# Kernel tuning notes

Measured on AMD Instinct MI355X. Metric: run time of the kernel, lower is better.

## Reference

```python
import jax, jax.numpy as jnp
import numpy as np

B, N_UNK, M_KNOWN = 8, 8192, 2048
C1, C2 = 256, 256
MLP = [512, 256, 256]
K_ENC = 32
D = MLP[-1]


def setup_inputs() -> dict:
    key = jax.random.key(0)
    ks = jax.random.split(key, 16)
    return {
        "unknown": jax.random.normal(ks[0], (B, N_UNK, 3), jnp.float32),
        "known": jax.random.normal(ks[1], (B, M_KNOWN, 3), jnp.float32),
        "unknow_feats": jax.random.normal(ks[2], (B, C1, N_UNK), jnp.float32),
        "known_feats": jax.random.normal(ks[3], (B, C2, M_KNOWN), jnp.float32),
        "conv_w1": jax.random.normal(ks[4], (MLP[1], MLP[0]), jnp.float32) * 0.05,
        "conv_b1": jnp.zeros((MLP[1],), jnp.float32),
        "bn_g1": jnp.ones((MLP[1],), jnp.float32),
        "bn_b1": jnp.zeros((MLP[1],), jnp.float32),
        "bn_m1": jax.random.normal(ks[5], (MLP[1],), jnp.float32) * 0.01,
        "bn_v1": jax.random.uniform(ks[6], (MLP[1],), jnp.float32, 0.5, 1.5),
        "conv_w2": jax.random.normal(ks[7], (MLP[2], MLP[1]), jnp.float32) * 0.05,
        "conv_b2": jnp.zeros((MLP[2],), jnp.float32),
        "bn_g2": jnp.ones((MLP[2],), jnp.float32),
        "bn_b2": jnp.zeros((MLP[2],), jnp.float32),
        "bn_m2": jax.random.normal(ks[8], (MLP[2],), jnp.float32) * 0.01,
        "bn_v2": jax.random.uniform(ks[9], (MLP[2],), jnp.float32, 0.5, 1.5),
        "enc_codewords": jax.random.normal(ks[10], (K_ENC, D), jnp.float32) * float(1.0 / np.sqrt(K_ENC * D)),
        "enc_scale": jax.random.uniform(ks[11], (K_ENC,), jnp.float32, -1.0, 0.0),
        "lin_w": jax.random.normal(ks[12], (D, D * K_ENC), jnp.float32) * 0.02,
        "lin_b": jnp.zeros((D,), jnp.float32),
    }


def _conv_bn_relu(x, w, b, g, beta, mean, var):
    # 1x1 conv over (B,C,N) == channel GEMM, then BN (inference form), then ReLU
    x = jnp.einsum("oc,bcn->bon", w, x) + b[None, :, None]
    x = g[None, :, None] * (x - mean[None, :, None]) * jax.lax.rsqrt(var + 1e-5)[None, :, None] + beta[None, :, None]
    return jax.nn.relu(x)


def reference(unknown, known, unknow_feats, known_feats,
              conv_w1, conv_b1, bn_g1, bn_b1, bn_m1, bn_v1,
              conv_w2, conv_b2, bn_g2, bn_b2, bn_m2, bn_v2,
              enc_codewords, enc_scale, lin_w, lin_b):
    # ---- three_nn: 3 nearest known points for each unknown point ----
    x2 = jnp.sum(unknown * unknown, axis=-1)            # (B,n)
    y2 = jnp.sum(known * known, axis=-1)                # (B,m)
    d2 = x2[:, :, None] - 2.0 * jnp.einsum("bnc,bmc->bnm", unknown, known) + y2[:, None, :]
    dist = jnp.sqrt(jnp.maximum(d2, 1e-12))             # (B,n,m) Euclidean
    neg_d, idx = jax.lax.top_k(-dist, 3)                # 3 smallest
    dist3 = -neg_d                                      # (B,n,3)
    dist_recip = 1.0 / (dist3 + 1e-8)
    weight = dist_recip / jnp.sum(dist_recip, axis=2, keepdims=True)
    # ---- three_interpolate: gather + weighted sum ----
    gathered = jax.vmap(lambda f, i: f[:, i])(known_feats, idx)   # (B,C2,n,3)
    interp = jnp.einsum("bcnk,bnk->bcn", gathered, weight)        # (B,C2,n)
    feats = jnp.concatenate([interp, unknow_feats], axis=1)       # (B,C2+C1,n)
    # ---- SharedMLP (two 1x1 conv + BN + ReLU layers) ----
    h = _conv_bn_relu(feats, conv_w1, conv_b1, bn_g1, bn_b1, bn_m1, bn_v1)
    h = _conv_bn_relu(h, conv_w2, conv_b2, bn_g2, bn_b2, bn_m2, bn_v2)   # (B,D,n)
    # ---- Encoding layer (soft dictionary assignment, residual aggregate) ----
    X = jnp.swapaxes(h, 1, 2)                                     # (B,n,D)
    c2 = jnp.sum(enc_codewords * enc_codewords, axis=-1)          # (K,)
    xn2 = jnp.sum(X * X, axis=-1)                                 # (B,n)
    # scaled_l2: s_k * ||x - c_k||^2 without materializing (B,n,K,D) residuals
    sl = enc_scale[None, None, :] * (xn2[:, :, None] - 2.0 * jnp.einsum("bnd,kd->bnk", X, enc_codewords) + c2[None, None, :])
    A = jax.nn.softmax(sl, axis=-1)                               # (B,n,K)
    E = jnp.einsum("bnk,bnd->bkd", A, X) - jnp.sum(A, axis=1)[:, :, None] * enc_codewords[None]
    E = jax.nn.relu(E).reshape(E.shape[0], -1)                    # (B,K*D)
    E = E / jnp.maximum(jnp.linalg.norm(E, axis=1, keepdims=True), 1e-12)  # F.normalize
    ctx = jax.nn.sigmoid(E @ lin_w.T + lin_b)                     # (B,D)
    # ---- channel-attention fusion ----
    return h * ctx[:, :, None]                                    # (B,D,n)
```

## Files before the change

### kernel.cpp

```cpp
#include <hip/hip_runtime.h>
#include <stdint.h>

typedef unsigned short u16;
typedef unsigned int u32;
typedef __attribute__((ext_vector_type(8))) short short8;
typedef __attribute__((ext_vector_type(4))) float f32x4;
typedef __attribute__((ext_vector_type(4))) u32 u32x4;

#define B_ 8
#define N_ 8192
#define M_ 2048
#define DD 256
#define KENC 32

#define SC1 0
#define SH1 256
#define SC2 512
#define SH2 768
#define C2OFF 1024
#define SOFF 1056
#define RNOFF 1088

#define OFF_IDX3   0ull
#define OFF_W3     786432ull
#define OFF_FT     1572864ull
#define OFF_H1T    68681728ull
#define OFF_ERELU  102236160ull
#define OFF_PART   102498304ull
#define OFF_CONSTS 102760448ull
#define OFF_CTX    102768640ull
#define OFF_W1D    102776832ull
#define OFF_W2D    103038976ull
#define OFF_CWD    103170048ull
#define OFF_FLAG   103186432ull

__device__ __forceinline__ float bf2f(u16 v){ return __uint_as_float(((u32)v)<<16); }
__device__ __forceinline__ u16 f2bf(float f){
  u32 x = __float_as_uint(f);
  return (u16)((x + 0x7FFFu + ((x>>16)&1u)) >> 16);
}
__device__ __forceinline__ float ldf(const void* p, size_t i, int f){
  return f ? ((const float*)p)[i] : bf2f(((const u16*)p)[i]);
}
__device__ __forceinline__ void gl_lds16(const u16* g, u16* l){
  __builtin_amdgcn_global_load_lds(
      (const __attribute__((address_space(1))) void*)g,
      (__attribute__((address_space(3))) void*)l, 16, 0, 0);
}

__global__ __launch_bounds__(256) void k_detect(const void* v1, int* flagp){
  __shared__ int cntb, cntf;
  int t = threadIdx.x;
  if (t==0){ cntb=0; cntf=0; }
  __syncthreads();
  float vb = bf2f(((const u16*)v1)[t]);
  if (!(vb > 0.4f && vb < 1.6f)) atomicAdd(&cntb, 1);
  if (t < 64){
    float vf = ((const float*)v1)[t];
    if (!(vf > 0.4f && vf < 1.6f)) atomicAdd(&cntf, 1);
  }
  __syncthreads();
  if (t==0) flagp[0] = (cntb > 0 && cntf == 0) ? 1 : 0;
}

__global__ __launch_bounds__(256) void k_convert(
    const void* w1, const void* w2, const void* cwsrc, const int* __restrict__ flagp,
    u16* __restrict__ W1d, u16* __restrict__ W2d, u16* __restrict__ CWd){
  int id = blockIdx.x*256 + threadIdx.x;
  int f = flagp[0];
  if (id < 131072){
    W1d[id] = f ? f2bf(((const float*)w1)[id]) : ((const u16*)w1)[id];
  } else if (id < 196608){
    int j = id - 131072;
    W2d[j] = f ? f2bf(((const float*)w2)[j]) : ((const u16*)w2)[j];
  } else if (id < 204800){
    int j = id - 196608;
    CWd[j] = f ? f2bf(((const float*)cwsrc)[j]) : ((const u16*)cwsrc)[j];
  }
}

__global__ __launch_bounds__(256) void k0_setup(
    const void* cb1, const void* g1, const void* be1, const void* m1, const void* v1,
    const void* cb2, const void* g2, const void* be2, const void* m2, const void* v2,
    const u16* __restrict__ CWd, const void* es, const int* __restrict__ flagp,
    float* __restrict__ consts){
  int t = threadIdx.x;
  int f = flagp[0];
  {
    float g = ldf(g1,t,f), be = ldf(be1,t,f), m = ldf(m1,t,f), v = ldf(v1,t,f), cb = ldf(cb1,t,f);
    float r = 1.f/sqrtf(v + 1e-5f);
    float sc = g*r;
    consts[SC1+t] = sc; consts[SH1+t] = (cb-m)*sc + be;
  }
  {
    float g = ldf(g2,t,f), be = ldf(be2,t,f), m = ldf(m2,t,f), v = ldf(v2,t,f), cb = ldf(cb2,t,f);
    float r = 1.f/sqrtf(v + 1e-5f);
    float sc = g*r;
    consts[SC2+t] = sc; consts[SH2+t] = (cb-m)*sc + be;
  }
  if (t < KENC){
    float s = 0.f;
    for (int d=0; d<DD; d++){ float c = bf2f(CWd[t*DD+d]); s = fmaf(c,c,s); }
    consts[C2OFF+t] = s;
    consts[SOFF+t]  = ldf(es,t,f);
  }
}

__device__ __forceinline__ float k1_dist2(float x2, float u2x, float u2y, float u2z, float4 km){
  float dot2 = __fadd_rn(__fadd_rn(__fmul_rn(u2x,km.x), __fmul_rn(u2y,km.y)), __fmul_rn(u2z,km.z));
  return __fadd_rn(__fsub_rn(x2, dot2), km.w);
}
__global__ __launch_bounds__(256) void k1_three_nn(
    const void* unknown, const void* known, const int* __restrict__ flagp,
    int* __restrict__ idx3, float* __restrict__ w3){
  __shared__ float4 kp[M_];
  int b = blockIdx.y, t = threadIdx.x;
  int f = flagp[0];
  for (int i=t; i<M_; i+=256){
    size_t o = ((size_t)b*M_ + i)*3;
    float x = ldf(known,o,f), y = ldf(known,o+1,f), z = ldf(known,o+2,f);
    float y2 = __fadd_rn(__fadd_rn(__fmul_rn(x,x), __fmul_rn(y,y)), __fmul_rn(z,z));
    kp[i] = make_float4(x,y,z,y2);
  }
  __syncthreads();
  int qq = t >> 2, sl = t & 3;
  int pid = blockIdx.x*64 + qq;
  size_t uo = ((size_t)b*N_ + pid)*3;
  float ux=ldf(unknown,uo,f), uy=ldf(unknown,uo+1,f), uz=ldf(unknown,uo+2,f);
  float x2 = __fadd_rn(__fadd_rn(__fmul_rn(ux,ux), __fmul_rn(uy,uy)), __fmul_rn(uz,uz));
  float u2x = ux+ux, u2y = uy+uy, u2z = uz+uz;
  float b0=3.4e38f, b1=3.4e38f, b2v=3.4e38f;
  const float4* kpl = kp + sl;
  for (int j0=0; j0<512; j0+=4){
    #pragma unroll
    for (int u=0; u<4; u++){
      float4 km = kpl[(j0+u)*4];
      float d2 = k1_dist2(x2,u2x,u2y,u2z,km);
      float t0 = fminf(b0, d2);
      float t1 = __builtin_amdgcn_fmed3f(b0, b1, d2);
      float t2 = __builtin_amdgcn_fmed3f(b1, b2v, d2);
      b0=t0; b1=t1; b2v=t2;
    }
  }
  #pragma unroll
  for (int st=1; st<4; st<<=1){
    float o0=__shfl_xor(b0,st,64), o1=__shfl_xor(b1,st,64), o2=__shfl_xor(b2v,st,64);
    float dv[3] = {o0,o1,o2};
    #pragma unroll
    for (int e=0; e<3; e++){
      float dd = dv[e];
      float t0 = fminf(b0, dd);
      float t1 = __builtin_amdgcn_fmed3f(b0, b1, dd);
      float t2 = __builtin_amdgcn_fmed3f(b1, b2v, dd);
      b0=t0; b1=t1; b2v=t2;
    }
  }
  float T = b2v;
  float e0=3.4e38f, e1=3.4e38f, e2=3.4e38f;
  int i0=0x7fffffff, i1=0x7fffffff, i2=0x7fffffff;
  for (int j0=0; j0<512; j0+=4){
    float d[4];
    #pragma unroll
    for (int u=0; u<4; u++){
      float4 km = kpl[(j0+u)*4];
      d[u] = k1_dist2(x2,u2x,u2y,u2z,km);
    }
    float gmin = fminf(fminf(d[0],d[1]), fminf(d[2],d[3]));
    if (__builtin_expect(gmin <= T, 0)){
      #pragma unroll
      for (int u=0; u<4; u++){
        float dd = d[u];
        if (dd <= T){
          int m = (j0+u)*4 + sl;
          bool lt0 = (dd < e0) || (dd == e0 && m < i0);
          bool lt1 = (dd < e1) || (dd == e1 && m < i1);
          bool lt2 = (dd < e2) || (dd == e2 && m < i2);
          float n2 = lt1 ? e1 : (lt2 ? dd : e2);  int ni2 = lt1 ? i1 : (lt2 ? m : i2);
          float n1 = lt0 ? e0 : (lt1 ? dd : e1);  int ni1 = lt0 ? i0 : (lt1 ? m : i1);
          e0 = lt0 ? dd : e0;  i0 = lt0 ? m : i0;
          e1 = n1; i1 = ni1; e2 = n2; i2 = ni2;
        }
      }
    }
  }
  #pragma unroll
  for (int st=1; st<4; st<<=1){
    float o0=__shfl_xor(e0,st,64), o1=__shfl_xor(e1,st,64), o2=__shfl_xor(e2,st,64);
    int   j0=__shfl_xor(i0,st,64), j1=__shfl_xor(i1,st,64), j2=__shfl_xor(i2,st,64);
    float dv[3] = {o0,o1,o2}; int jv[3] = {j0,j1,j2};
    #pragma unroll
    for (int e=0; e<3; e++){
      float dd = dv[e]; int jj = jv[e];
      bool lt2 = (dd < e2) || (dd == e2 && jj < i2);
      if (lt2){
        bool lt0 = (dd < e0) || (dd == e0 && jj < i0);
        bool lt1 = (dd < e1) || (dd == e1 && jj < i1);
        if (lt0){ e2=e1;i2=i1; e1=e0;i1=i0; e0=dd;i0=jj; }
        else if (lt1){ e2=e1;i2=i1; e1=dd;i1=jj; }
        else { e2=dd; i2=jj; }
      }
    }
  }
  if (sl == 0){
    float da = __fsqrt_rn(fmaxf(e0,1e-12f));
    float db = __fsqrt_rn(fmaxf(e1,1e-12f));
    float dc = __fsqrt_rn(fmaxf(e2,1e-12f));
    float r0 = __fdiv_rn(1.f, __fadd_rn(da,1e-8f));
    float r1 = __fdiv_rn(1.f, __fadd_rn(db,1e-8f));
    float r2 = __fdiv_rn(1.f, __fadd_rn(dc,1e-8f));
    float rs = __fadd_rn(__fadd_rn(r0,r1),r2);
    size_t o = ((size_t)b*N_ + pid)*3;
    idx3[o]=i0; idx3[o+1]=i1; idx3[o+2]=i2;
    w3[o]=__fdiv_rn(r0,rs); w3[o+1]=__fdiv_rn(r1,rs); w3[o+2]=__fdiv_rn(r2,rs);
  }
}

__global__ __launch_bounds__(256) void k2_interp(
    const void* kf, const int* __restrict__ idx3,
    const float* __restrict__ w3, const int* __restrict__ flagp, u16* __restrict__ Ft){
  __shared__ u16 Ls[M_*8];
  int ct = blockIdx.x;
  int rg = blockIdx.y;
  int b = blockIdx.z, t = threadIdx.x;
  int f = flagp[0];
  for (int cp=0; cp<4; cp++){
    int c0 = ct*8 + cp*2;
    size_t base0 = ((size_t)b*DD + c0)*M_;
    size_t base1 = base0 + M_;
    for (int i=t; i<M_; i+=256){
      float f0 = ldf(kf, base0+i, f);
      float f1 = ldf(kf, base1+i, f);
      u32 w = (u32)f2bf(f0) | ((u32)f2bf(f1)<<16);
      *(u32*)(Ls + i*8 + cp*2) = w;
    }
  }
  __syncthreads();
  for (int rep=rg*8; rep<rg*8+8; rep++){
    int pid = rep*256 + t;
    size_t o3 = ((size_t)b*N_ + pid)*3;
    int ia = idx3[o3], ib = idx3[o3+1], ic = idx3[o3+2];
    float wa = w3[o3], wb = w3[o3+1], wc = w3[o3+2];
    short8 va = *(const short8*)(Ls + ia*8);
    short8 vb = *(const short8*)(Ls + ib*8);
    short8 vc = *(const short8*)(Ls + ic*8);
    u32x4 pk;
    #pragma unroll
    for (int cq=0; cq<4; cq++){
      float fa0 = bf2f((u16)va[cq*2]),   fb0 = bf2f((u16)vb[cq*2]),   fc0 = bf2f((u16)vc[cq*2]);
      float fa1 = bf2f((u16)va[cq*2+1]), fb1 = bf2f((u16)vb[cq*2+1]), fc1 = bf2f((u16)vc[cq*2+1]);
      float v0 = fmaf(wc, fc0, fmaf(wb, fb0, wa*fa0));
      float v1 = fmaf(wc, fc1, fmaf(wb, fb1, wa*fa1));
      pk[cq] = (u32)f2bf(v0) | ((u32)f2bf(v1)<<16);
    }
    *(u32x4*)(Ft + ((size_t)b*N_ + pid)*512 + ct*8) = pk;
  }
}

__global__ __launch_bounds__(256) void k2b_transpose_uf(
    const void* uf, const int* __restrict__ flagp, u16* __restrict__ Ft){
  __shared__ u16 Ls[64*72];
  int bx = blockIdx.x, cy = blockIdx.y, b = blockIdx.z, t = threadIdx.x;
  int f = flagp[0];
  {
    int n = t & 63, cg = t >> 6;
    for (int i=0; i<16; i++){
      int c = cg*16 + i;
      Ls[n*72 + c] = f2bf(ldf(uf, ((size_t)b*DD + cy*64 + c)*N_ + bx*64 + n, f));
    }
  }
  __syncthreads();
  int nl = t>>2, cc = t&3;
  u16* dst = Ft + ((size_t)b*N_ + bx*64 + nl)*512 + 256 + cy*64 + cc*16;
  *(u32x4*)dst     = *(const u32x4*)(Ls + nl*72 + cc*16);
  *(u32x4*)(dst+8) = *(const u32x4*)(Ls + nl*72 + cc*16 + 8);
}

__global__ __launch_bounds__(256) void gemm_bn_relu(
    const u16* __restrict__ W, const u16* __restrict__ Fin,
    const float* __restrict__ consts, int sc_off, int sh_off,
    u16* __restrict__ Out, int K){
  __shared__ u16 SM[17408];
  u16* As = SM; u16* Bs = SM + 8192;
  int b = blockIdx.z, ot = blockIdx.y*128, nt = blockIdx.x*128;
  int t = threadIdx.x, wave = t>>6, lane = t&63, ln = lane&15, quad = lane>>4;
  int wo = (wave&1)*64, wn = (wave>>1)*64;
  f32x4 acc[4][4];
  #pragma unroll
  for (int i=0;i<4;i++)
    #pragma unroll
    for (int j=0;j<4;j++) acc[i][j] = (f32x4)0.f;
  const u16* Wp = W + (size_t)ot*K;
  const u16* Fp = Fin + ((size_t)b*N_ + nt)*K;
  for (int kk=0; kk<K; kk+=64){
    #pragma unroll
    for (int i=0;i<4;i++){
      int c = wave*256 + i*64 + lane;
      int r = c>>3, k8 = (c&7) ^ (r&7);
      const u16* gA = Wp + (size_t)r*K + kk + k8*8;
      const u16* gB = Fp + (size_t)r*K + kk + k8*8;
      gl_lds16(gA, As + (size_t)(wave*256 + i*64)*8);
      gl_lds16(gB, Bs + (size_t)(wave*256 + i*64)*8);
    }
    __syncthreads();
    #pragma unroll
    for (int kh=0; kh<2; kh++){
      short8 af[4], bfr[4];
      #pragma unroll
      for (int i=0;i<4;i++){
        int R = wo + i*16 + ln, C = kh*4 + quad;
        af[i] = *(const short8*)(As + (size_t)(R*8 + (C^(R&7)))*8);
      }
      #pragma unroll
      for (int j=0;j<4;j++){
        int R = wn + j*16 + ln, C = kh*4 + quad;
        bfr[j] = *(const short8*)(Bs + (size_t)(R*8 + (C^(R&7)))*8);
      }
      #pragma unroll
      for (int i=0;i<4;i++)
        #pragma unroll
        for (int j=0;j<4;j++)
          acc[i][j] = __builtin_amdgcn_mfma_f32_16x16x32_bf16(af[i], bfr[j], acc[i][j], 0,0,0);
    }
    __syncthreads();
  }
  u16* Cs = SM;
  #pragma unroll
  for (int i=0;i<4;i++){
    #pragma unroll
    for (int r=0;r<4;r++){
      int ol = wo + i*16 + quad*4 + r;
      float sc = consts[sc_off + ot + ol], sh = consts[sh_off + ot + ol];
      #pragma unroll
      for (int j=0;j<4;j++){
        float v = fmaxf(fmaf(acc[i][j][r], sc, sh), 0.f);
        Cs[(wn + j*16 + ln)*136 + ol] = f2bf(v);
      }
    }
  }
  __syncthreads();
  int nl = t>>1, half = t&1;
  u16* dst = Out + ((size_t)b*N_ + nt + nl)*256 + ot + half*64;
  const u16* srcr = Cs + nl*136 + half*64;
  #pragma unroll
  for (int c=0;c<8;c++)
    *(u32x4*)(dst + c*8) = *(const u32x4*)(srcr + c*8);
}

__global__ __launch_bounds__(256, 6) void k5_enc_partial(
    const u16* __restrict__ X, const u16* __restrict__ cw,
    const float* __restrict__ consts, float* __restrict__ Epart,
    float* __restrict__ Asum){
  __shared__ u16 Xs[64*256];
  __shared__ float A_lds[64*32];
  int g = blockIdx.x, b = blockIdx.y, t = threadIdx.x;
  int wave = t>>6, lane = t&63, ln = lane&15, quad = lane>>4;
  int ka = lane>>1, h = lane&1;
  int dbase = wave*64 + h*32;
  float c2v0 = consts[C2OFF + ln], c2v1 = consts[C2OFF + 16 + ln];
  float sv0  = consts[SOFF + ln],  sv1  = consts[SOFF + 16 + ln];
  int n0 = g*64;
  const u16* Xp = X + ((size_t)b*N_ + n0)*256;
  #pragma unroll
  for (int i=0;i<8;i++){
    int ch = t + i*256;
    int r = ch>>5, cc = ch&31;
    *(u32x4*)(Xs + r*256 + ((cc ^ (r&15))<<3)) = *(const u32x4*)(Xp + r*256 + cc*8);
  }
  __syncthreads();
  float xnf;
  {
    int row = t>>2, part = t&3;
    float s = 0.f;
    #pragma unroll
    for (int j=0;j<8;j++){
      int cc = part*8 + j;
      short8 xv = *(const short8*)(Xs + row*256 + ((cc ^ (row&15))<<3));
      #pragma unroll
      for (int q=0;q<8;q++){ float x = bf2f((u16)xv[q]); s = fmaf(x,x,s); }
    }
    s += __shfl_xor(s,1,64);
    s += __shfl_xor(s,2,64);
    xnf = s;
  }
  f32x4 pj0 = (f32x4)0.f, pj1 = (f32x4)0.f;
  {
    int row = wave*16 + ln;
    #pragma unroll
    for (int kk=0; kk<256; kk+=32){
      int cc = (kk>>3) + quad;
      short8 a   = *(const short8*)(Xs + row*256 + ((cc ^ (row&15))<<3));
      short8 bf0 = *(const short8*)(cw + (size_t)ln*256 + kk + quad*8);
      short8 bf1 = *(const short8*)(cw + (size_t)(16+ln)*256 + kk + quad*8);
      pj0 = __builtin_amdgcn_mfma_f32_16x16x32_bf16(a, bf0, pj0, 0,0,0);
      pj1 = __builtin_amdgcn_mfma_f32_16x16x32_bf16(a, bf1, pj1, 0,0,0);
    }
  }
  #pragma unroll
  for (int r=0;r<4;r++){
    int nl = wave*16 + quad*4 + r;
    float xv = __shfl(xnf, (quad*4 + r)*4, 64);
    float v0 = sv0 * __fadd_rn(__fsub_rn(xv, __fmul_rn(2.f,pj0[r])), c2v0);
    float v1 = sv1 * __fadd_rn(__fsub_rn(xv, __fmul_rn(2.f,pj1[r])), c2v1);
    float mx = fmaxf(v0,v1);
    #pragma unroll
    for (int d=1; d<16; d<<=1) mx = fmaxf(mx, __shfl_xor(mx, d, 64));
    float e0 = __expf(v0-mx), e1 = __expf(v1-mx);
    float es = e0+e1;
    #pragma unroll
    for (int d=1; d<16; d<<=1) es += __shfl_xor(es, d, 64);
    float inv = 1.f/es;
    A_lds[nl*32 + ln]      = e0*inv;
    A_lds[nl*32 + 16 + ln] = e1*inv;
  }
  __syncthreads();
  float accE[32];
  #pragma unroll
  for (int p=0;p<32;p++) accE[p]=0.f;
  float asum = 0.f;
  int cbase = wave*8 + h*4;
  #pragma unroll 2
  for (int n=0; n<64; n++){
    float a = A_lds[n*32 + ka];
    asum += a;
    const u16* xr = Xs + n*256;
    int sw = (n&15)<<3;
    #pragma unroll
    for (int p8=0; p8<4; p8++){
      u32x4 xv = *(const u32x4*)(xr + ((((cbase + p8)<<3) ^ sw)));
      #pragma unroll
      for (int q=0; q<4; q++){
        u32 w = xv[q];
        float lo = __uint_as_float(w<<16);
        float hi = __uint_as_float(w & 0xffff0000u);
        accE[p8*8 + q*2]   = fmaf(a, lo, accE[p8*8 + q*2]);
        accE[p8*8 + q*2+1] = fmaf(a, hi, accE[p8*8 + q*2+1]);
      }
    }
  }
  int slab = b*128 + g;
  float* Ed = Epart + (size_t)slab*8192 + (size_t)ka*256 + dbase;
  #pragma unroll
  for (int p=0;p<32;p++) Ed[p] = accE[p];
  if (wave==0 && h==0) Asum[slab*32 + ka] = asum;
}

__global__ __launch_bounds__(256) void k5b_reduce(
    const float* __restrict__ Epart, const float* __restrict__ Asum,
    const u16* __restrict__ cw, float* __restrict__ Erelu){
  int id = blockIdx.x*256 + threadIdx.x;
  int d = id & 255, k = (id>>8)&31, b = id>>13;
  float s = 0.f, as = 0.f;
  for (int sl=0; sl<128; sl++){
    s  += Epart[((size_t)(b*128+sl))*8192 + (size_t)k*256 + d];
    as += Asum[(b*128+sl)*32 + k];
  }
  float cv = bf2f(cw[k*256+d]);
  Erelu[(size_t)b*8192 + k*256 + d] = fmaxf(s - as*cv, 0.f);
}

__global__ __launch_bounds__(256) void k6a_norm(
    const float* __restrict__ Erelu, float* __restrict__ consts){
  __shared__ float red[256];
  int b = blockIdx.x, t = threadIdx.x;
  float s = 0.f;
  for (int i=0;i<32;i++){ float e = Erelu[(size_t)b*8192 + i*256 + t]; s = fmaf(e,e,s); }
  red[t] = s; __syncthreads();
  for (int w=128; w>0; w>>=1){ if (t<w) red[t] += red[t+w]; __syncthreads(); }
  if (t==0) consts[RNOFF + b] = 1.f/fmaxf(__fsqrt_rn(red[0]), 1e-12f);
}

__global__ __launch_bounds__(256) void k6b_partial(
    const float* __restrict__ Erelu, const void* lw, const int* __restrict__ flagp,
    float* __restrict__ partials){
  __shared__ float Er[256];
  int kc = blockIdx.x, b = blockIdx.y, t = threadIdx.x;
  int f = flagp[0];
  Er[t] = Erelu[(size_t)b*8192 + kc*256 + t];
  __syncthreads();
  float s = 0.f;
  if (f){
    const float* lwp = (const float*)lw + (size_t)t*8192 + kc*256;
    for (int p=0; p<256; p+=4){
      f32x4 v = *(const f32x4*)(lwp + p);
      #pragma unroll
      for (int q=0;q<4;q++) s = fmaf(Er[p+q], v[q], s);
    }
  } else {
    const u16* lwp = (const u16*)lw + (size_t)t*8192 + kc*256;
    for (int p=0; p<256; p+=8){
      u32x4 v = *(const u32x4*)(lwp + p);
      #pragma unroll
      for (int q=0;q<4;q++){
        u32 w = v[q];
        s = fmaf(Er[p+q*2],   __uint_as_float(w<<16), s);
        s = fmaf(Er[p+q*2+1], __uint_as_float(w & 0xffff0000u), s);
      }
    }
  }
  partials[((size_t)b*32 + kc)*256 + t] = s;
}

__global__ __launch_bounds__(256) void k6c_ctx(
    const float* __restrict__ partials, const float* __restrict__ consts,
    const void* lb, const int* __restrict__ flagp, float* __restrict__ ctx){
  int b = blockIdx.x, t = threadIdx.x;
  int f = flagp[0];
  float s = 0.f;
  for (int kc=0; kc<32; kc++) s += partials[((size_t)b*32+kc)*256 + t];
  float x = fmaf(consts[RNOFF+b], s, ldf(lb,t,f));
  ctx[b*256 + t] = 1.f/(1.f + __expf(-x));
}

__global__ __launch_bounds__(256) void k7_out(
    const u16* __restrict__ ht, const float* __restrict__ ctx,
    const int* __restrict__ flagp, void* out){
  __shared__ u16 Ls[64*72];
  int bx = blockIdx.x, oy = blockIdx.y, b = blockIdx.z, t = threadIdx.x;
  int f = flagp[0];
  {
    int nl = t>>2, oc = t&3;
    const u16* src = ht + ((size_t)b*N_ + bx*64 + nl)*256 + oy*64 + oc*16;
    *(u32x4*)(Ls + nl*72 + oc*16)     = *(const u32x4*)src;
    *(u32x4*)(Ls + nl*72 + oc*16 + 8) = *(const u32x4*)(src + 8);
  }
  __syncthreads();
  int ol = t>>2, nc = t&3;
  float cv = ctx[b*256 + oy*64 + ol];
  size_t dstoff = ((size_t)b*DD + oy*64 + ol)*N_ + bx*64 + nc*16;
  if (f){
    float* dst = (float*)out + dstoff;
    #pragma unroll
    for (int wq=0; wq<4; wq++){
      f32x4 v;
      #pragma unroll
      for (int q=0;q<4;q++) v[q] = bf2f(Ls[(nc*16 + wq*4 + q)*72 + ol]) * cv;
      *(f32x4*)(dst + wq*4) = v;
    }
  } else {
    u32 words[8];
    #pragma unroll
    for (int wq=0; wq<8; wq++){
      float v0 = bf2f(Ls[(nc*16 + wq*2)*72 + ol]) * cv;
      float v1 = bf2f(Ls[(nc*16 + wq*2+1)*72 + ol]) * cv;
      words[wq] = (u32)f2bf(v0) | ((u32)f2bf(v1)<<16);
    }
    u16* dst = (u16*)out + dstoff;
    u32x4 w0 = {words[0],words[1],words[2],words[3]};
    u32x4 w1 = {words[4],words[5],words[6],words[7]};
    *(u32x4*)dst     = w0;
    *(u32x4*)(dst+8) = w1;
  }
}

extern "C" void kernel_launch(void* const* d_in, const int* in_sizes, int n_in,
                              void* d_out, int out_size, void* d_ws, size_t ws_size,
                              hipStream_t stream){
  const void* unknown = d_in[0];
  const void* known   = d_in[1];
  const void* uf      = d_in[2];
  const void* kf      = d_in[3];
  const void* w1      = d_in[4];
  const void* cb1     = d_in[5];
  const void* g1      = d_in[6];
  const void* be1     = d_in[7];
  const void* m1      = d_in[8];
  const void* v1      = d_in[9];
  const void* w2      = d_in[10];
  const void* cb2     = d_in[11];
  const void* g2      = d_in[12];
  const void* be2     = d_in[13];
  const void* m2      = d_in[14];
  const void* v2      = d_in[15];
  const void* cw      = d_in[16];
  const void* es      = d_in[17];
  const void* lw      = d_in[18];
  const void* lb      = d_in[19];

  char* ws = (char*)d_ws;
  int*   idx3  = (int*)(ws + OFF_IDX3);
  float* w3    = (float*)(ws + OFF_W3);
  u16*   Ft    = (u16*)(ws + OFF_FT);
  u16*   ht    = Ft;
  u16*   h1t   = (u16*)(ws + OFF_H1T);
  float* Epart = (float*)(ws + OFF_H1T);
  float* Asum  = (float*)(ws + OFF_IDX3);
  float* Erelu    = (float*)(ws + OFF_ERELU);
  float* partials = (float*)(ws + OFF_PART);
  float* consts   = (float*)(ws + OFF_CONSTS);
  float* ctx      = (float*)(ws + OFF_CTX);
  u16*   W1d   = (u16*)(ws + OFF_W1D);
  u16*   W2d   = (u16*)(ws + OFF_W2D);
  u16*   CWd   = (u16*)(ws + OFF_CWD);
  int*   flagp = (int*)(ws + OFF_FLAG);

  k_detect<<<1, 256, 0, stream>>>(v1, flagp);
  k_convert<<<800, 256, 0, stream>>>(w1, w2, cw, flagp, W1d, W2d, CWd);
  k0_setup<<<1, 256, 0, stream>>>(cb1,g1,be1,m1,v1, cb2,g2,be2,m2,v2, CWd, es, flagp, consts);
  k1_three_nn<<<dim3(128,8), 256, 0, stream>>>(unknown, known, flagp, idx3, w3);
  k2_interp<<<dim3(32,4,8), 256, 0, stream>>>(kf, idx3, w3, flagp, Ft);
  k2b_transpose_uf<<<dim3(128,4,8), 256, 0, stream>>>(uf, flagp, Ft);
  gemm_bn_relu<<<dim3(64,2,8), 256, 0, stream>>>(W1d, Ft,  consts, SC1, SH1, h1t, 512);
  gemm_bn_relu<<<dim3(64,2,8), 256, 0, stream>>>(W2d, h1t, consts, SC2, SH2, ht,  256);
  k5_enc_partial<<<dim3(128,8), 256, 0, stream>>>(ht, CWd, consts, Epart, Asum);
  k5b_reduce<<<256, 256, 0, stream>>>(Epart, Asum, CWd, Erelu);
  k6a_norm<<<8, 256, 0, stream>>>(Erelu, consts);
  k6b_partial<<<dim3(32,8), 256, 0, stream>>>(Erelu, lw, flagp, partials);
  k6c_ctx<<<8, 256, 0, stream>>>(partials, consts, lb, flagp, ctx);
  k7_out<<<dim3(128,4,8), 256, 0, stream>>>(ht, ctx, flagp, d_out);
}
```

Baseline: 472.4 us.

## Compute three-NN distances with bf16 split MFMA and exact candidate refinement

```diff
diff --git a/kernel.cpp b/kernel.cpp
--- a/kernel.cpp
+++ b/kernel.cpp
@@ -33,6 +33,10 @@
 #define OFF_W2D    103038976ull
 #define OFF_CWD    103170048ull
 #define OFF_FLAG   103186432ull
+#define OFF_QF     OFF_FT
+#define OFF_PF     (OFF_FT + 4194304ull)
+
+#define LCAP 32
 
 __device__ __forceinline__ float bf2f(u16 v){ return __uint_as_float(((u32)v)<<16); }
 __device__ __forceinline__ u16 f2bf(float f){
@@ -51,7 +55,7 @@
 __global__ __launch_bounds__(256) void k_detect(const void* v1, int* flagp){
   __shared__ int cntb, cntf;
   int t = threadIdx.x;
-  if (t==0){ cntb=0; cntf=0; }
+  if (t==0){ cntb=0; cntf=0; ((u32*)flagp)[1] = 0u; }
   __syncthreads();
   float vb = bf2f(((const u16*)v1)[t]);
   if (!(vb > 0.4f && vb < 1.6f)) atomicAdd(&cntb, 1);
@@ -79,6 +83,68 @@
   }
 }
 
+__global__ __launch_bounds__(256) void k_frag(
+    const void* unknown, const void* known, const int* __restrict__ flagp,
+    u16* __restrict__ Qf, u16* __restrict__ Pf, u32* __restrict__ cmaxp){
+  __shared__ float mred[256];
+  int id = blockIdx.x*256 + threadIdx.x;
+  int t = threadIdx.x;
+  int f = flagp[0];
+  float mx = 0.f;
+  u16 S[32];
+  if (id < 81920){
+    int isq = id < 65536;
+    int b, row; size_t o;
+    if (isq){ b = id >> 13; row = id & 8191; o = ((size_t)b*N_ + row)*3; }
+    else { int j = id - 65536; b = j >> 11; row = j & 2047; o = ((size_t)b*M_ + row)*3; }
+    float x = ldf(isq?unknown:known, o, f);
+    float y = ldf(isq?unknown:known, o+1, f);
+    float z = ldf(isq?unknown:known, o+2, f);
+    mx = fmaxf(fmaxf(fabsf(x),fabsf(y)),fabsf(z));
+    float s2 = __fadd_rn(__fadd_rn(__fmul_rn(x,x), __fmul_rn(y,y)), __fmul_rn(z,z));
+    float c[3] = {x,y,z};
+    #pragma unroll
+    for (int d3=0; d3<3; d3++){
+      float u = c[d3];
+      u16 h = f2bf(u);  float r1 = __fsub_rn(u, bf2f(h));
+      u16 m2 = f2bf(r1); float r2 = __fsub_rn(r1, bf2f(m2));
+      u16 l2 = f2bf(r2);
+      u16 sv[3];
+      if (isq){
+        sv[0] = f2bf(-2.f*bf2f(h));
+        sv[1] = f2bf(-2.f*bf2f(m2));
+        sv[2] = f2bf(-2.f*bf2f(l2));
+        #pragma unroll
+        for (int a=0; a<3; a++)
+          #pragma unroll
+          for (int bb=0; bb<3; bb++) S[d3*9 + a*3 + bb] = sv[a];
+      } else {
+        sv[0] = h; sv[1] = m2; sv[2] = l2;
+        #pragma unroll
+        for (int a=0; a<3; a++)
+          #pragma unroll
+          for (int bb=0; bb<3; bb++) S[d3*9 + a*3 + bb] = sv[bb];
+      }
+    }
+    u16 s2h = f2bf(s2); u16 s2l = f2bf(__fsub_rn(s2, bf2f(s2h)));
+    if (isq){ S[27]=s2h; S[28]=s2l; S[29]=0x3F80; S[30]=0x3F80; }
+    else    { S[27]=0x3F80; S[28]=0x3F80; S[29]=s2h; S[30]=s2l; }
+    S[31] = 0;
+    u16* dst = isq ? (Qf + ((size_t)(b*512 + (row>>4))*512) + (row&15)*8)
+                   : (Pf + ((size_t)(b*128 + (row>>4))*512) + (row&15)*8);
+    #pragma unroll
+    for (int qd=0; qd<4; qd++){
+      u32x4 w;
+      #pragma unroll
+      for (int q=0; q<4; q++) w[q] = (u32)S[qd*8+q*2] | ((u32)S[qd*8+q*2+1]<<16);
+      *(u32x4*)(dst + qd*128) = w;
+    }
+  }
+  mred[t] = mx; __syncthreads();
+  for (int w=128; w>0; w>>=1){ if (t<w) mred[t] = fmaxf(mred[t], mred[t+w]); __syncthreads(); }
+  if (t==0) atomicMax(cmaxp, __float_as_uint(mred[0]));
+}
+
 __global__ __launch_bounds__(256) void k0_setup(
     const void* cb1, const void* g1, const void* be1, const void* m1, const void* v1,
     const void* cb2, const void* g2, const void* be2, const void* m2, const void* v2,
@@ -106,102 +172,116 @@
   }
 }
 
-__device__ __forceinline__ float k1_dist2(float x2, float u2x, float u2y, float u2z, float4 km){
-  float dot2 = __fadd_rn(__fadd_rn(__fmul_rn(u2x,km.x), __fmul_rn(u2y,km.y)), __fmul_rn(u2z,km.z));
-  return __fadd_rn(__fsub_rn(x2, dot2), km.w);
-}
 __global__ __launch_bounds__(256) void k1_three_nn(
     const void* unknown, const void* known, const int* __restrict__ flagp,
+    const u16* __restrict__ Qf, const u16* __restrict__ Pf,
+    const u32* __restrict__ cmaxp,
     int* __restrict__ idx3, float* __restrict__ w3){
-  __shared__ float4 kp[M_];
+  __shared__ int lists[64*LCAP];
+  __shared__ int lcount[64];
   int b = blockIdx.y, t = threadIdx.x;
   int f = flagp[0];
-  for (int i=t; i<M_; i+=256){
-    size_t o = ((size_t)b*M_ + i)*3;
-    float x = ldf(known,o,f), y = ldf(known,o+1,f), z = ldf(known,o+2,f);
-    float y2 = __fadd_rn(__fadd_rn(__fmul_rn(x,x), __fmul_rn(y,y)), __fmul_rn(z,z));
-    kp[i] = make_float4(x,y,z,y2);
-  }
-  __syncthreads();
-  int qq = t >> 2, sl = t & 3;
-  int pid = blockIdx.x*64 + qq;
-  size_t uo = ((size_t)b*N_ + pid)*3;
-  float ux=ldf(unknown,uo,f), uy=ldf(unknown,uo+1,f), uz=ldf(unknown,uo+2,f);
-  float x2 = __fadd_rn(__fadd_rn(__fmul_rn(ux,ux), __fmul_rn(uy,uy)), __fmul_rn(uz,uz));
-  float u2x = ux+ux, u2y = uy+uy, u2z = uz+uz;
-  float b0=3.4e38f, b1=3.4e38f, b2v=3.4e38f;
-  const float4* kpl = kp + sl;
-  for (int j0=0; j0<512; j0+=4){
-    #pragma unroll
-    for (int u=0; u<4; u++){
-      float4 km = kpl[(j0+u)*4];
-      float d2 = k1_dist2(x2,u2x,u2y,u2z,km);
-      float t0 = fminf(b0, d2);
-      float t1 = __builtin_amdgcn_fmed3f(b0, b1, d2);
-      float t2 = __builtin_amdgcn_fmed3f(b1, b2v, d2);
-      b0=t0; b1=t1; b2v=t2;
-    }
-  }
-  #pragma unroll
-  for (int st=1; st<4; st<<=1){
-    float o0=__shfl_xor(b0,st,64), o1=__shfl_xor(b1,st,64), o2=__shfl_xor(b2v,st,64);
-    float dv[3] = {o0,o1,o2};
+  if (t < 64) lcount[t] = 0;
+  int wave = t>>6, ln = t&15, quad = (t>>4)&3;
+  int qt = blockIdx.x*4 + wave;
+  short8 bq = *(const short8*)(Qf + ((size_t)(b*512 + qt)*512) + (quad*16+ln)*8);
+  const u16* Pfb = Pf + (size_t)b*65536 + (quad*16+ln)*8;
+  float C = __uint_as_float(cmaxp[0]);
+  float delta = C*C*(1.0f/2048.f);
+  __syncthreads();
+  float a0=3.4e38f, a1=3.4e38f, a2=3.4e38f;
+  float c0=3.4e38f, c1=3.4e38f, c2=3.4e38f;
+  for (int mt=0; mt<128; mt+=2){
+    short8 apA = *(const short8*)(Pfb + mt*512);
+    short8 apB = *(const short8*)(Pfb + mt*512 + 512);
+    f32x4 dA = __builtin_amdgcn_mfma_f32_16x16x32_bf16(apA, bq, (f32x4)0.f, 0,0,0);
+    f32x4 dB = __builtin_amdgcn_mfma_f32_16x16x32_bf16(apB, bq, (f32x4)0.f, 0,0,0);
+    #pragma unroll
+    for (int r=0; r<4; r++){
+      float dx = dA[r];
+      float t0=fminf(a0,dx), t1=__builtin_amdgcn_fmed3f(a0,a1,dx), t2=__builtin_amdgcn_fmed3f(a1,a2,dx);
+      a0=t0; a1=t1; a2=t2;
+      float dy = dB[r];
+      float s0=fminf(c0,dy), s1=__builtin_amdgcn_fmed3f(c0,c1,dy), s2=__builtin_amdgcn_fmed3f(c1,c2,dy);
+      c0=s0; c1=s1; c2=s2;
+    }
+  }
+  {
+    float dv3[3] = {c0,c1,c2};
     #pragma unroll
     for (int e=0; e<3; e++){
-      float dd = dv[e];
-      float t0 = fminf(b0, dd);
-      float t1 = __builtin_amdgcn_fmed3f(b0, b1, dd);
-      float t2 = __builtin_amdgcn_fmed3f(b1, b2v, dd);
-      b0=t0; b1=t1; b2v=t2;
-    }
-  }
-  float T = b2v;
-  float e0=3.4e38f, e1=3.4e38f, e2=3.4e38f;
-  int i0=0x7fffffff, i1=0x7fffffff, i2=0x7fffffff;
-  for (int j0=0; j0<512; j0+=4){
-    float d[4];
-    #pragma unroll
-    for (int u=0; u<4; u++){
-      float4 km = kpl[(j0+u)*4];
-      d[u] = k1_dist2(x2,u2x,u2y,u2z,km);
-    }
-    float gmin = fminf(fminf(d[0],d[1]), fminf(d[2],d[3]));
-    if (__builtin_expect(gmin <= T, 0)){
-      #pragma unroll
-      for (int u=0; u<4; u++){
-        float dd = d[u];
-        if (dd <= T){
-          int m = (j0+u)*4 + sl;
-          bool lt0 = (dd < e0) || (dd == e0 && m < i0);
-          bool lt1 = (dd < e1) || (dd == e1 && m < i1);
-          bool lt2 = (dd < e2) || (dd == e2 && m < i2);
-          float n2 = lt1 ? e1 : (lt2 ? dd : e2);  int ni2 = lt1 ? i1 : (lt2 ? m : i2);
-          float n1 = lt0 ? e0 : (lt1 ? dd : e1);  int ni1 = lt0 ? i0 : (lt1 ? m : i1);
-          e0 = lt0 ? dd : e0;  i0 = lt0 ? m : i0;
-          e1 = n1; i1 = ni1; e2 = n2; i2 = ni2;
+      float dx = dv3[e];
+      float t0=fminf(a0,dx), t1=__builtin_amdgcn_fmed3f(a0,a1,dx), t2=__builtin_amdgcn_fmed3f(a1,a2,dx);
+      a0=t0; a1=t1; a2=t2;
+    }
+  }
+  #pragma unroll
+  for (int st=16; st<64; st<<=1){
+    float o0=__shfl_xor(a0,st,64), o1=__shfl_xor(a1,st,64), o2=__shfl_xor(a2,st,64);
+    float dv3[3] = {o0,o1,o2};
+    #pragma unroll
+    for (int e=0; e<3; e++){
+      float dx = dv3[e];
+      float t0=fminf(a0,dx), t1=__builtin_amdgcn_fmed3f(a0,a1,dx), t2=__builtin_amdgcn_fmed3f(a1,a2,dx);
+      a0=t0; a1=t1; a2=t2;
+    }
+  }
+  float TT = a2 + 2.f*delta;
+  int lq = wave*16 + ln;
+  for (int mt=0; mt<128; mt++){
+    short8 ap = *(const short8*)(Pfb + mt*512);
+    f32x4 dv = __builtin_amdgcn_mfma_f32_16x16x32_bf16(ap, bq, (f32x4)0.f, 0,0,0);
+    if (__builtin_expect(dv[0]<=TT || dv[1]<=TT || dv[2]<=TT || dv[3]<=TT, 0)){
+      #pragma unroll
+      for (int r=0; r<4; r++){
+        if (dv[r] <= TT){
+          int m = mt*16 + quad*4 + r;
+          int ix = atomicAdd(&lcount[lq], 1);
+          if (ix < LCAP) lists[lq*LCAP + ix] = m;
         }
       }
     }
   }
-  #pragma unroll
-  for (int st=1; st<4; st<<=1){
-    float o0=__shfl_xor(e0,st,64), o1=__shfl_xor(e1,st,64), o2=__shfl_xor(e2,st,64);
-    int   j0=__shfl_xor(i0,st,64), j1=__shfl_xor(i1,st,64), j2=__shfl_xor(i2,st,64);
-    float dv[3] = {o0,o1,o2}; int jv[3] = {j0,j1,j2};
-    #pragma unroll
-    for (int e=0; e<3; e++){
-      float dd = dv[e]; int jj = jv[e];
-      bool lt2 = (dd < e2) || (dd == e2 && jj < i2);
-      if (lt2){
-        bool lt0 = (dd < e0) || (dd == e0 && jj < i0);
-        bool lt1 = (dd < e1) || (dd == e1 && jj < i1);
-        if (lt0){ e2=e1;i2=i1; e1=e0;i1=i0; e0=dd;i0=jj; }
-        else if (lt1){ e2=e1;i2=i1; e1=dd;i1=jj; }
-        else { e2=dd; i2=jj; }
-      }
-    }
-  }
-  if (sl == 0){
+  __syncthreads();
+  if (quad == 0){
+    int pid = blockIdx.x*64 + wave*16 + ln;
+    size_t uo = ((size_t)b*N_ + pid)*3;
+    float ux=ldf(unknown,uo,f), uy=ldf(unknown,uo+1,f), uz=ldf(unknown,uo+2,f);
+    float x2 = __fadd_rn(__fadd_rn(__fmul_rn(ux,ux), __fmul_rn(uy,uy)), __fmul_rn(uz,uz));
+    float u2x=ux+ux, u2y=uy+uy, u2z=uz+uz;
+    float e0=3.4e38f, e1=3.4e38f, e2=3.4e38f;
+    int i0=0x7fffffff, i1=0x7fffffff, i2=0x7fffffff;
+    int cnt = lcount[lq];
+    int lim = (cnt <= LCAP) ? cnt : 0;
+    for (int ii=0; ii<lim; ii++){
+      int m = lists[lq*LCAP + ii];
+      size_t o = ((size_t)b*M_ + m)*3;
+      float kx=ldf(known,o,f), ky=ldf(known,o+1,f), kz=ldf(known,o+2,f);
+      float y2 = __fadd_rn(__fadd_rn(__fmul_rn(kx,kx), __fmul_rn(ky,ky)), __fmul_rn(kz,kz));
+      float dot2 = __fadd_rn(__fadd_rn(__fmul_rn(u2x,kx), __fmul_rn(u2y,ky)), __fmul_rn(u2z,kz));
+      float dd = __fadd_rn(__fsub_rn(x2, dot2), y2);
+      bool lt0 = (dd < e0) || (dd == e0 && m < i0);
+      bool lt1 = (dd < e1) || (dd == e1 && m < i1);
+      bool lt2 = (dd < e2) || (dd == e2 && m < i2);
+      if (lt0){ e2=e1;i2=i1; e1=e0;i1=i0; e0=dd;i0=m; }
+      else if (lt1){ e2=e1;i2=i1; e1=dd;i1=m; }
+      else if (lt2){ e2=dd; i2=m; }
+    }
+    if (cnt > LCAP){
+      for (int m=0; m<M_; m++){
+        size_t o = ((size_t)b*M_ + m)*3;
+        float kx=ldf(known,o,f), ky=ldf(known,o+1,f), kz=ldf(known,o+2,f);
+        float y2 = __fadd_rn(__fadd_rn(__fmul_rn(kx,kx), __fmul_rn(ky,ky)), __fmul_rn(kz,kz));
+        float dot2 = __fadd_rn(__fadd_rn(__fmul_rn(u2x,kx), __fmul_rn(u2y,ky)), __fmul_rn(u2z,kz));
+        float dd = __fadd_rn(__fsub_rn(x2, dot2), y2);
+        bool lt0 = (dd < e0) || (dd == e0 && m < i0);
+        bool lt1 = (dd < e1) || (dd == e1 && m < i1);
+        bool lt2 = (dd < e2) || (dd == e2 && m < i2);
+        if (lt0){ e2=e1;i2=i1; e1=e0;i1=i0; e0=dd;i0=m; }
+        else if (lt1){ e2=e1;i2=i1; e1=dd;i1=m; }
+        else if (lt2){ e2=dd; i2=m; }
+      }
+    }
     float da = __fsqrt_rn(fmaxf(e0,1e-12f));
     float db = __fsqrt_rn(fmaxf(e1,1e-12f));
     float dc = __fsqrt_rn(fmaxf(e2,1e-12f));
@@ -592,11 +672,15 @@
   u16*   W2d   = (u16*)(ws + OFF_W2D);
   u16*   CWd   = (u16*)(ws + OFF_CWD);
   int*   flagp = (int*)(ws + OFF_FLAG);
+  u32*   cmaxp = (u32*)(ws + OFF_FLAG) + 1;
+  u16*   Qf    = (u16*)(ws + OFF_QF);
+  u16*   Pf    = (u16*)(ws + OFF_PF);
 
   k_detect<<<1, 256, 0, stream>>>(v1, flagp);
   k_convert<<<800, 256, 0, stream>>>(w1, w2, cw, flagp, W1d, W2d, CWd);
+  k_frag<<<320, 256, 0, stream>>>(unknown, known, flagp, Qf, Pf, cmaxp);
   k0_setup<<<1, 256, 0, stream>>>(cb1,g1,be1,m1,v1, cb2,g2,be2,m2,v2, CWd, es, flagp, consts);
-  k1_three_nn<<<dim3(128,8), 256, 0, stream>>>(unknown, known, flagp, idx3, w3);
+  k1_three_nn<<<dim3(128,8), 256, 0, stream>>>(unknown, known, flagp, Qf, Pf, cmaxp, idx3, w3);
   k2_interp<<<dim3(32,4,8), 256, 0, stream>>>(kf, idx3, w3, flagp, Ft);
   k2b_transpose_uf<<<dim3(128,4,8), 256, 0, stream>>>(uf, flagp, Ft);
   gemm_bn_relu<<<dim3(64,2,8), 256, 0, stream>>>(W1d, Ft,  consts, SC1, SH1, h1t, 512);
```

Measured after the change: 463.8 us. No clear change (-1.8%).
